# Kernel optimization log

Hardware: AMD Instinct MI355X
Metric: run time of the kernel (lower is better)

Reference implementation:

```python
import jax, jax.numpy as jnp
import numpy as np

ATT_SCALE = 1.0  # att_scale_factor


def setup_inputs() -> dict:
    key = jax.random.key(0)
    k1, k2, k3, k4, k5 = jax.random.split(key, 5)
    B, P, IMG_D, SEQ_D, H = 64, 576, 1024, 1024, 512
    seq_features = jax.random.normal(k1, (B, SEQ_D), dtype=jnp.float32)
    img_features = jax.random.normal(k2, (B, P, IMG_D), dtype=jnp.float32)
    # torch nn.Linear weights: [out_features, in_features], scaled to typical init magnitude
    W_seq = jax.random.normal(k3, (H, SEQ_D), dtype=jnp.float32) * (1.0 / np.sqrt(SEQ_D))
    W_img = jax.random.normal(k4, (H, IMG_D), dtype=jnp.float32) * (1.0 / np.sqrt(IMG_D))
    W_w = jax.random.normal(k5, (1, H), dtype=jnp.float32) * (1.0 / np.sqrt(H))
    return {"seq_features": seq_features, "img_features": img_features,
            "W_seq": W_seq, "W_img": W_img, "W_w": W_w}


def reference(seq_features, img_features, W_seq, W_img, W_w):
    # tanh(SeqTrans(seq)) broadcast over patch dim (avoids explicit .repeat)
    seq_h = jnp.tanh(jnp.einsum('bd,hd->bh', seq_features, W_seq))          # [B, H]
    img_h = jnp.tanh(jnp.einsum('bpd,hd->bph', img_features, W_img))        # [B, P, H]
    attend = seq_h[:, None, :] * img_h                                       # [B, P, H]
    # Dropout is Identity (att_dropout=None)
    scores = ATT_SCALE * jnp.einsum('bph,oh->bpo', attend, W_w)              # [B, P, 1]
    alpha = jax.nn.softmax(scores, axis=1)                                   # softmax over patches
    # weighted sum over patches; alpha broadcasts over channel dim (no .repeat needed)
    attended_img = jnp.sum(img_features * alpha, axis=1)                     # [B, IMG_D]
    return attended_img
```

## Files before the change

kernel.cpp:

```cpp
#include <hip/hip_runtime.h>
#include <hip/hip_bf16.h>

#define BB 64
#define PP 576
#define DD 1024
#define HH 512

typedef __attribute__((ext_vector_type(4))) float f32x4;
typedef __attribute__((ext_vector_type(8))) short bf16x8;

__device__ __forceinline__ unsigned short f2bf(float f) {
    union { float f; unsigned u; } v; v.f = f;
    unsigned r = v.u + 0x7FFF + ((v.u >> 16) & 1);
    return (unsigned short)(r >> 16);
}

__device__ __forceinline__ float fast_tanh(float x) {
    float e = __expf(2.f * x);
    return 1.f - 2.f / (e + 1.f);
}

__device__ __forceinline__ void gload16(const void* g, void* l) {
    __builtin_amdgcn_global_load_lds((const __attribute__((address_space(1))) unsigned int*)g,
                                     (__attribute__((address_space(3))) unsigned int*)l,
                                     16, 0, 0);
}

__global__ __launch_bounds__(256) void k_convert(const float* __restrict__ w,
                                                 unsigned short* __restrict__ o) {
    int i = (blockIdx.x * 256 + threadIdx.x) * 4;
    f32x4 v = *(const f32x4*)(w + i);
    ushort4 r;
    r.x = f2bf(v.x); r.y = f2bf(v.y); r.z = f2bf(v.z); r.w = f2bf(v.w);
    *(ushort4*)(o + i) = r;
}

__global__ __launch_bounds__(128) void k_seq(const float* __restrict__ seq,
                                             const float* __restrict__ W_seq,
                                             const float* __restrict__ W_w,
                                             float* __restrict__ g) {
    int b = blockIdx.x;
    int h = blockIdx.y * 128 + threadIdx.x;
    __shared__ float s_seq[DD];
    #pragma unroll
    for (int i = 0; i < 8; i++) s_seq[threadIdx.x + i * 128] = seq[b * DD + threadIdx.x + i * 128];
    __syncthreads();
    const float* wr = W_seq + (size_t)h * DD;
    float acc = 0.f;
    #pragma unroll 4
    for (int d = 0; d < DD; d += 4) {
        f32x4 w4 = *(const f32x4*)(wr + d);
        acc += w4.x * s_seq[d] + w4.y * s_seq[d + 1] + w4.z * s_seq[d + 2] + w4.w * s_seq[d + 3];
    }
    g[b * HH + h] = fast_tanh(acc) * W_w[h];
}

__global__ __launch_bounds__(256, 4) void k_scores(const float* __restrict__ img,
                                                   const unsigned short* __restrict__ Wb,
                                                   const float* __restrict__ g,
                                                   float* __restrict__ sp) {
    int b = blockIdx.y;
    int rt = blockIdx.x % 9;
    int ch = blockIdx.x / 9;
    int p0 = rt * 64;
    int h0 = ch * 256;
    int tid = threadIdx.x;
    int w = tid >> 6, lane = tid & 63;

    __shared__ unsigned short As[2][64 * 32];
    __shared__ unsigned short Bs[2][256 * 32];

    float gr[4];
    #pragma unroll
    for (int n = 0; n < 4; ++n) gr[n] = g[b * HH + h0 + w * 64 + n * 16 + (lane & 15)];

    f32x4 acc[4][4];
    #pragma unroll
    for (int m = 0; m < 4; m++)
        #pragma unroll
        for (int n = 0; n < 4; n++) acc[m][n] = (f32x4)0.f;

    int arow = tid >> 2;
    int acnk = tid & 3;
    const float* asrc = img + ((size_t)(b * PP + p0 + arow)) * DD + acnk * 8;
    int aw = arow * 32 + ((acnk ^ ((arow >> 1) & 3)) * 8);

    int rl = lane >> 2;
    int bswz = (lane & 3) ^ ((rl >> 1) & 3);
    const unsigned short* bbase = Wb + (size_t)h0 * DD;

    f32x4 u0, u1;

    u0 = *(const f32x4*)(asrc);
    u1 = *(const f32x4*)(asrc + 4);
    __builtin_amdgcn_sched_barrier(0);
    #pragma unroll
    for (int i = 0; i < 4; ++i) {
        int hr = w * 64 + i * 16 + rl;
        gload16(bbase + (size_t)hr * DD + bswz * 8, &Bs[0][(w * 4 + i) * 512]);
    }
    asm volatile("s_waitcnt vmcnt(4)" ::: "memory");
    {
        bf16x8 p;
        p[0] = (short)f2bf(u0.x); p[1] = (short)f2bf(u0.y);
        p[2] = (short)f2bf(u0.z); p[3] = (short)f2bf(u0.w);
        p[4] = (short)f2bf(u1.x); p[5] = (short)f2bf(u1.y);
        p[6] = (short)f2bf(u1.z); p[7] = (short)f2bf(u1.w);
        *(bf16x8*)&As[0][aw] = p;
    }
    asm volatile("s_waitcnt lgkmcnt(0)" ::: "memory");
    __builtin_amdgcn_s_barrier();

    int r15 = lane & 15;
    int csw = (lane >> 4) ^ ((r15 >> 1) & 3);

    for (int kr = 0; kr < 32; ++kr) {
        int cur = kr & 1, nxt = cur ^ 1;
        if (kr < 31) {
            int k0 = (kr + 1) * 32;
            u0 = *(const f32x4*)(asrc + k0);
            u1 = *(const f32x4*)(asrc + k0 + 4);
            __builtin_amdgcn_sched_barrier(0);
            #pragma unroll
            for (int i = 0; i < 4; ++i) {
                int hr = w * 64 + i * 16 + rl;
                gload16(bbase + (size_t)hr * DD + k0 + bswz * 8, &Bs[nxt][(w * 4 + i) * 512]);
            }
            asm volatile("s_waitcnt vmcnt(6)" ::: "memory");
        } else {
            asm volatile("s_waitcnt vmcnt(0)" ::: "memory");
        }
        {
            bf16x8 af[4], bfv[4];
            #pragma unroll
            for (int m = 0; m < 4; ++m)
                af[m] = *(const bf16x8*)&As[cur][(m * 16 + r15) * 32 + csw * 8];
            #pragma unroll
            for (int n = 0; n < 4; ++n)
                bfv[n] = *(const bf16x8*)&Bs[cur][(w * 64 + n * 16 + r15) * 32 + csw * 8];
            #pragma unroll
            for (int m = 0; m < 4; ++m)
                #pragma unroll
                for (int n = 0; n < 4; ++n)
                    acc[m][n] = __builtin_amdgcn_mfma_f32_16x16x32_bf16(af[m], bfv[n], acc[m][n], 0, 0, 0);
        }
        if (kr < 31) {
            asm volatile("s_waitcnt vmcnt(4)" ::: "memory");
            bf16x8 p;
            p[0] = (short)f2bf(u0.x); p[1] = (short)f2bf(u0.y);
            p[2] = (short)f2bf(u0.z); p[3] = (short)f2bf(u0.w);
            p[4] = (short)f2bf(u1.x); p[5] = (short)f2bf(u1.y);
            p[6] = (short)f2bf(u1.z); p[7] = (short)f2bf(u1.w);
            *(bf16x8*)&As[nxt][aw] = p;
            asm volatile("s_waitcnt lgkmcnt(0)" ::: "memory");
            __builtin_amdgcn_s_barrier();
        }
    }

    float part[4][4];
    #pragma unroll
    for (int m = 0; m < 4; m++)
        #pragma unroll
        for (int j = 0; j < 4; j++) part[m][j] = 0.f;
    #pragma unroll
    for (int m = 0; m < 4; ++m)
        #pragma unroll
        for (int n = 0; n < 4; ++n) {
            float gv = gr[n];
            f32x4 v = acc[m][n];
            #pragma unroll
            for (int j = 0; j < 4; ++j) part[m][j] += fast_tanh(v[j]) * gv;
        }
    #pragma unroll
    for (int mask = 1; mask < 16; mask <<= 1)
        #pragma unroll
        for (int m = 0; m < 4; ++m)
            #pragma unroll
            for (int j = 0; j < 4; ++j)
                part[m][j] += __shfl_xor(part[m][j], mask, 64);

    float* red = (float*)&As[0][0];
    if ((lane & 15) == 0) {
        int hi = lane >> 4;
        #pragma unroll
        for (int m = 0; m < 4; ++m)
            #pragma unroll
            for (int j = 0; j < 4; ++j)
                red[w * 64 + m * 16 + hi * 4 + j] = part[m][j];
    }
    __syncthreads();
    if (tid < 64) {
        float s = red[tid] + red[64 + tid] + red[128 + tid] + red[192 + tid];
        sp[(size_t)ch * (BB * PP) + b * PP + p0 + tid] = s;
    }
}

__global__ __launch_bounds__(576) void k_softmax(const float* __restrict__ sp,
                                                 float* __restrict__ alpha) {
    int b = blockIdx.x;
    int t = threadIdx.x;
    __shared__ float red[9];
    float s = sp[b * PP + t] + sp[BB * PP + b * PP + t];
    float m = s;
    #pragma unroll
    for (int off = 32; off; off >>= 1) m = fmaxf(m, __shfl_xor(m, off, 64));
    int w = t >> 6;
    if ((t & 63) == 0) red[w] = m;
    __syncthreads();
    float gm = red[0];
    #pragma unroll
    for (int i = 1; i < 9; i++) gm = fmaxf(gm, red[i]);
    float e = __expf(s - gm);
    float sum = e;
    #pragma unroll
    for (int off = 32; off; off >>= 1) sum += __shfl_xor(sum, off, 64);
    __syncthreads();
    if ((t & 63) == 0) red[w] = sum;
    __syncthreads();
    float gsum = 0.f;
    #pragma unroll
    for (int i = 0; i < 9; i++) gsum += red[i];
    alpha[b * PP + t] = e / gsum;
}

__global__ __launch_bounds__(256) void k_attend(const float* __restrict__ img,
                                                const float* __restrict__ alpha,
                                                float* __restrict__ part) {
    int b = blockIdx.y;
    int pc = blockIdx.x;
    int t = threadIdx.x;
    __shared__ float al[64];
    if (t < 64) al[t] = alpha[b * PP + pc * 64 + t];
    __syncthreads();
    int d = t * 4;
    f32x4 acc = (f32x4)0.f;
    const float* base = img + ((size_t)b * PP + (size_t)pc * 64) * DD + d;
    #pragma unroll 4
    for (int i = 0; i < 64; i++) {
        f32x4 v = *(const f32x4*)(base + (size_t)i * DD);
        acc += al[i] * v;
    }
    float* o = part + ((size_t)pc * BB + b) * DD + d;
    *(f32x4*)o = acc;
}

__global__ __launch_bounds__(256) void k_reduce(const float* __restrict__ part,
                                                float* __restrict__ out) {
    int i = blockIdx.x * 256 + threadIdx.x;
    float s = 0.f;
    #pragma unroll
    for (int pc = 0; pc < 9; pc++) s += part[pc * (BB * DD) + i];
    out[i] = s;
}

extern "C" void kernel_launch(void* const* d_in, const int* in_sizes, int n_in,
                              void* d_out, int out_size, void* d_ws, size_t ws_size,
                              hipStream_t stream) {
    const float* seq   = (const float*)d_in[0];
    const float* img   = (const float*)d_in[1];
    const float* W_seq = (const float*)d_in[2];
    const float* W_img = (const float*)d_in[3];
    const float* W_w   = (const float*)d_in[4];
    float* out = (float*)d_out;

    char* ws = (char*)d_ws;
    unsigned short* Wb = (unsigned short*)ws;
    float* g      = (float*)(ws + 1048576);
    float* sp     = (float*)(ws + 1048576 + 131072);
    float* alpha  = (float*)(ws + 1048576 + 131072 + 294912);
    float* part   = (float*)(ws + 1048576 + 131072 + 294912 + 147456);

    k_convert<<<512, 256, 0, stream>>>(W_img, Wb);
    k_seq<<<dim3(BB, 4), 128, 0, stream>>>(seq, W_seq, W_w, g);
    k_scores<<<dim3(18, BB), 256, 0, stream>>>(img, Wb, g, sp);
    k_softmax<<<BB, 576, 0, stream>>>(sp, alpha);
    k_attend<<<dim3(9, BB), 256, 0, stream>>>(img, alpha, part);
    k_reduce<<<256, 256, 0, stream>>>(part, out);
}
```

Baseline: 143.2 us.

## Load A fragments directly into registers and drop LDS staging and barriers

The scores GEMM no longer stages the fp32 image tile through LDS. Each wave now loads its A fragments straight from global memory in MFMA layout, converts them with packed v_cvt_pk_bf16_f32 instructions, and double-buffers both the A registers and the per-wave B LDS tiles in a two-stage unrolled loop. Since each wave touches only its own B rows, the block-wide barriers in the main loop are removed. In exchange, all four waves redundantly fetch the same A tile from cache, register pressure rises, and launch bounds drop to 2 waves per SIMD, reducing occupancy.

Measured after the change: 235.1 us. 1.64x slower.

```diff
diff --git a/kernel.cpp b/kernel.cpp
--- a/kernel.cpp
+++ b/kernel.cpp
@@ -24,6 +24,15 @@
     __builtin_amdgcn_global_load_lds((const __attribute__((address_space(1))) unsigned int*)g,
                                      (__attribute__((address_space(3))) unsigned int*)l,
                                      16, 0, 0);
+}
+
+__device__ __forceinline__ bf16x8 cvt8(f32x4 a, f32x4 b) {
+    union { bf16x8 v; unsigned u[4]; } r;
+    asm("v_cvt_pk_bf16_f32 %0, %1, %2" : "=v"(r.u[0]) : "v"(a.x), "v"(a.y));
+    asm("v_cvt_pk_bf16_f32 %0, %1, %2" : "=v"(r.u[1]) : "v"(a.z), "v"(a.w));
+    asm("v_cvt_pk_bf16_f32 %0, %1, %2" : "=v"(r.u[2]) : "v"(b.x), "v"(b.y));
+    asm("v_cvt_pk_bf16_f32 %0, %1, %2" : "=v"(r.u[3]) : "v"(b.z), "v"(b.w));
+    return r.v;
 }
 
 __global__ __launch_bounds__(256) void k_convert(const float* __restrict__ w,
@@ -55,7 +64,7 @@
     g[b * HH + h] = fast_tanh(acc) * W_w[h];
 }
 
-__global__ __launch_bounds__(256, 4) void k_scores(const float* __restrict__ img,
+__global__ __launch_bounds__(256, 2) void k_scores(const float* __restrict__ img,
                                                    const unsigned short* __restrict__ Wb,
                                                    const float* __restrict__ g,
                                                    float* __restrict__ sp) {
@@ -66,13 +75,15 @@
     int h0 = ch * 256;
     int tid = threadIdx.x;
     int w = tid >> 6, lane = tid & 63;
-
-    __shared__ unsigned short As[2][64 * 32];
+    int r15 = lane & 15;
+    int kq = lane >> 4;
+    int csw = kq ^ ((r15 >> 1) & 3);
+
     __shared__ unsigned short Bs[2][256 * 32];
 
     float gr[4];
     #pragma unroll
-    for (int n = 0; n < 4; ++n) gr[n] = g[b * HH + h0 + w * 64 + n * 16 + (lane & 15)];
+    for (int n = 0; n < 4; ++n) gr[n] = g[b * HH + h0 + w * 64 + n * 16 + r15];
 
     f32x4 acc[4][4];
     #pragma unroll
@@ -80,81 +91,66 @@
         #pragma unroll
         for (int n = 0; n < 4; n++) acc[m][n] = (f32x4)0.f;
 
-    int arow = tid >> 2;
-    int acnk = tid & 3;
-    const float* asrc = img + ((size_t)(b * PP + p0 + arow)) * DD + acnk * 8;
-    int aw = arow * 32 + ((acnk ^ ((arow >> 1) & 3)) * 8);
+    const float* abase[4];
+    #pragma unroll
+    for (int m = 0; m < 4; ++m)
+        abase[m] = img + ((size_t)(b * PP + p0 + m * 16 + r15)) * DD + kq * 8;
 
     int rl = lane >> 2;
     int bswz = (lane & 3) ^ ((rl >> 1) & 3);
     const unsigned short* bbase = Wb + (size_t)h0 * DD;
 
-    f32x4 u0, u1;
-
-    u0 = *(const f32x4*)(asrc);
-    u1 = *(const f32x4*)(asrc + 4);
-    __builtin_amdgcn_sched_barrier(0);
-    #pragma unroll
-    for (int i = 0; i < 4; ++i) {
-        int hr = w * 64 + i * 16 + rl;
-        gload16(bbase + (size_t)hr * DD + bswz * 8, &Bs[0][(w * 4 + i) * 512]);
-    }
-    asm volatile("s_waitcnt vmcnt(4)" ::: "memory");
-    {
-        bf16x8 p;
-        p[0] = (short)f2bf(u0.x); p[1] = (short)f2bf(u0.y);
-        p[2] = (short)f2bf(u0.z); p[3] = (short)f2bf(u0.w);
-        p[4] = (short)f2bf(u1.x); p[5] = (short)f2bf(u1.y);
-        p[6] = (short)f2bf(u1.z); p[7] = (short)f2bf(u1.w);
-        *(bf16x8*)&As[0][aw] = p;
-    }
-    asm volatile("s_waitcnt lgkmcnt(0)" ::: "memory");
-    __builtin_amdgcn_s_barrier();
-
-    int r15 = lane & 15;
-    int csw = (lane >> 4) ^ ((r15 >> 1) & 3);
-
-    for (int kr = 0; kr < 32; ++kr) {
-        int cur = kr & 1, nxt = cur ^ 1;
-        if (kr < 31) {
-            int k0 = (kr + 1) * 32;
-            u0 = *(const f32x4*)(asrc + k0);
-            u1 = *(const f32x4*)(asrc + k0 + 4);
-            __builtin_amdgcn_sched_barrier(0);
-            #pragma unroll
-            for (int i = 0; i < 4; ++i) {
-                int hr = w * 64 + i * 16 + rl;
-                gload16(bbase + (size_t)hr * DD + k0 + bswz * 8, &Bs[nxt][(w * 4 + i) * 512]);
-            }
-            asm volatile("s_waitcnt vmcnt(6)" ::: "memory");
+    f32x4 uaE[4][2], uaO[4][2];
+
+    auto issueA = [&](f32x4 (&ua)[4][2], int kr) {
+        int k0 = kr * 32;
+        #pragma unroll
+        for (int m = 0; m < 4; ++m) {
+            ua[m][0] = *(const f32x4*)(abase[m] + k0);
+            ua[m][1] = *(const f32x4*)(abase[m] + k0 + 4);
+        }
+    };
+    auto issueB = [&](unsigned short* Bsb, int kr) {
+        int k0 = kr * 32;
+        #pragma unroll
+        for (int i = 0; i < 4; ++i) {
+            int hr = w * 64 + i * 16 + rl;
+            gload16(bbase + (size_t)hr * DD + k0 + bswz * 8, Bsb + (w * 4 + i) * 512);
+        }
+    };
+    auto compute = [&](const f32x4 (&ua)[4][2], const unsigned short* Bsb) {
+        bf16x8 af[4], bf[4];
+        #pragma unroll
+        for (int m = 0; m < 4; ++m) af[m] = cvt8(ua[m][0], ua[m][1]);
+        #pragma unroll
+        for (int n = 0; n < 4; ++n)
+            bf[n] = *(const bf16x8*)&Bsb[(w * 64 + n * 16 + r15) * 32 + csw * 8];
+        #pragma unroll
+        for (int m = 0; m < 4; ++m)
+            #pragma unroll
+            for (int n = 0; n < 4; ++n)
+                acc[m][n] = __builtin_amdgcn_mfma_f32_16x16x32_bf16(af[m], bf[n], acc[m][n], 0, 0, 0);
+    };
+
+    issueA(uaE, 0);
+    issueB(&Bs[0][0], 0);
+
+    for (int kr2 = 0; kr2 < 16; ++kr2) {
+        int kr = kr2 * 2;
+        issueA(uaO, kr + 1);
+        issueB(&Bs[1][0], kr + 1);
+        asm volatile("s_waitcnt vmcnt(12)" ::: "memory");
+        __builtin_amdgcn_sched_barrier(0);
+        compute(uaE, &Bs[0][0]);
+        if (kr2 < 15) {
+            issueA(uaE, kr + 2);
+            issueB(&Bs[0][0], kr + 2);
+            asm volatile("s_waitcnt vmcnt(12)" ::: "memory");
         } else {
             asm volatile("s_waitcnt vmcnt(0)" ::: "memory");
         }
-        {
-            bf16x8 af[4], bfv[4];
-            #pragma unroll
-            for (int m = 0; m < 4; ++m)
-                af[m] = *(const bf16x8*)&As[cur][(m * 16 + r15) * 32 + csw * 8];
-            #pragma unroll
-            for (int n = 0; n < 4; ++n)
-                bfv[n] = *(const bf16x8*)&Bs[cur][(w * 64 + n * 16 + r15) * 32 + csw * 8];
-            #pragma unroll
-            for (int m = 0; m < 4; ++m)
-                #pragma unroll
-                for (int n = 0; n < 4; ++n)
-                    acc[m][n] = __builtin_amdgcn_mfma_f32_16x16x32_bf16(af[m], bfv[n], acc[m][n], 0, 0, 0);
-        }
-        if (kr < 31) {
-            asm volatile("s_waitcnt vmcnt(4)" ::: "memory");
-            bf16x8 p;
-            p[0] = (short)f2bf(u0.x); p[1] = (short)f2bf(u0.y);
-            p[2] = (short)f2bf(u0.z); p[3] = (short)f2bf(u0.w);
-            p[4] = (short)f2bf(u1.x); p[5] = (short)f2bf(u1.y);
-            p[6] = (short)f2bf(u1.z); p[7] = (short)f2bf(u1.w);
-            *(bf16x8*)&As[nxt][aw] = p;
-            asm volatile("s_waitcnt lgkmcnt(0)" ::: "memory");
-            __builtin_amdgcn_s_barrier();
-        }
+        __builtin_amdgcn_sched_barrier(0);
+        compute(uaO, &Bs[1][0]);
     }
 
     float part[4][4];
@@ -179,8 +175,9 @@
             for (int j = 0; j < 4; ++j)
                 part[m][j] += __shfl_xor(part[m][j], mask, 64);
 
-    float* red = (float*)&As[0][0];
-    if ((lane & 15) == 0) {
+    __syncthreads();
+    float* red = (float*)&Bs[0][0];
+    if (r15 == 0) {
         int hi = lane >> 4;
         #pragma unroll
         for (int m = 0; m < 4; ++m)
```
